# Performance work log

Hardware: AMD Instinct MI355X
Metric: run time of the kernel (lower is better)

## Reference

```python
import jax, jax.numpy as jnp
import numpy as np

N_HEAD = 16
NEG = -10000.0


def setup_inputs() -> dict:
    key = jax.random.key(0)
    k1, k2, k3 = jax.random.split(key, 3)
    B, S, NX = 2, 2048, 1024
    x = jax.random.normal(k1, (B, S, NX), dtype=jnp.float32)
    # Conv1D weights: y = x @ W + b (HF Conv1D stores weight as [in, out])
    w_attn = jax.random.normal(k2, (NX, 3 * NX), dtype=jnp.float32) * 0.02
    b_attn = jnp.zeros((3 * NX,), dtype=jnp.float32)
    w_proj = jax.random.normal(k3, (NX, NX), dtype=jnp.float32) * 0.02
    b_proj = jnp.zeros((NX,), dtype=jnp.float32)
    return {"x": x, "w_attn": w_attn, "b_attn": b_attn,
            "w_proj": w_proj, "b_proj": b_proj}


def reference(x, w_attn, b_attn, w_proj, b_proj):
    B, S, NX = x.shape
    H = N_HEAD
    D = NX // H  # head dim
    qkv = x @ w_attn + b_attn                      # [B, S, 3*NX]
    q, k, v = jnp.split(qkv, 3, axis=-1)
    # split heads -> [B, H, S, D]
    q = q.reshape(B, S, H, D).transpose(0, 2, 1, 3)
    k = k.reshape(B, S, H, D).transpose(0, 2, 1, 3)
    v = v.reshape(B, S, H, D).transpose(0, 2, 1, 3)
    # scores [B, H, S, S], scaled (scale=True)
    w = jnp.einsum('bhqd,bhkd->bhqk', q, k) / jnp.sqrt(jnp.asarray(D, x.dtype))
    # causal additive mask exactly as the torch code: w*b + NEG*(1-b)
    bias = jnp.tril(jnp.ones((S, S), dtype=x.dtype))[None, None]  # [1,1,S,S]
    w = w * bias + NEG * (1.0 - bias)
    w = jax.nn.softmax(w, axis=-1)
    a = jnp.einsum('bhqk,bhkd->bhqd', w, v)        # [B, H, S, D]
    a = a.transpose(0, 2, 1, 3).reshape(B, S, NX)  # merge heads
    return a @ w_proj + b_proj
```

## Files before the change

kernel.cpp:

```cpp
#include <hip/hip_runtime.h>
#include <cstdint>
#include <cstddef>


typedef __bf16 bf16;
typedef __bf16 bf16x8 __attribute__((ext_vector_type(8)));
typedef __bf16 bf16x4 __attribute__((ext_vector_type(4)));
typedef float f32x4 __attribute__((ext_vector_type(4)));
typedef float f32x16 __attribute__((ext_vector_type(16)));

#define MFMA16(a, b, c) __builtin_amdgcn_mfma_f32_16x16x32_bf16(a, b, c, 0, 0, 0)
#define MFMA32(a, b, c) __builtin_amdgcn_mfma_f32_32x32x16_bf16(a, b, c, 0, 0, 0)

typedef const __attribute__((address_space(1))) void* gas_ptr;
typedef __attribute__((address_space(3))) void* las_ptr;
__device__ __forceinline__ void async16(const void* g, void* l) {
    __builtin_amdgcn_global_load_lds((gas_ptr)g, (las_ptr)l, 16, 0, 0);
}
__device__ __forceinline__ float exp2f_fast(float x) { return __builtin_amdgcn_exp2f(x); }
__device__ __forceinline__ uint32_t pkbf(float a, float b) {
    union { bf16 x[2]; uint32_t u; } t;
    t.x[0] = (bf16)a; t.x[1] = (bf16)b;
    return t.u;
}

__global__ __launch_bounds__(256) void prep_kernel(const float* __restrict__ x, bf16* __restrict__ xb,
                                                   const float* __restrict__ wa, bf16* __restrict__ wTa,
                                                   const float* __restrict__ wp, bf16* __restrict__ wTp) {
    __shared__ float tile[32][33];
    const int bid = blockIdx.x, tid = threadIdx.x;
    if (bid < 4096) {
        int i = (bid * 256 + tid) * 4;
        float4 v = *reinterpret_cast<const float4*>(x + i);
        bf16x4 o;
        o[0] = (bf16)v.x; o[1] = (bf16)v.y; o[2] = (bf16)v.z; o[3] = (bf16)v.w;
        *reinterpret_cast<bf16x4*>(xb + i) = o;
        return;
    }
    const float* in; bf16* out; int N, t;
    if (bid < 7168) { t = bid - 4096; in = wa; out = wTa; N = 3072; }
    else            { t = bid - 7168; in = wp; out = wTp; N = 1024; }
    const int K = 1024;
    int bx = t % (N >> 5), by = t / (N >> 5);
    int n0 = bx * 32, k0 = by * 32, tx = tid & 31, ty = tid >> 5;
#pragma unroll
    for (int i = 0; i < 32; i += 8)
        tile[ty + i][tx] = in[(size_t)(k0 + ty + i) * N + n0 + tx];
    __syncthreads();
#pragma unroll
    for (int i = 0; i < 32; i += 8)
        out[(size_t)(n0 + ty + i) * K + k0 + tx] = (bf16)tile[tx][ty + i];
}

template <int OUT_BF16>
__global__ __launch_bounds__(256) void gemm_kernel(const bf16* __restrict__ A,
                                                   const bf16* __restrict__ Bt,
                                                   const float* __restrict__ bias,
                                                   void* __restrict__ Cout,
                                                   int M, int N, int K) {
    __shared__ bf16 Alds[2][128 * 32];
    __shared__ bf16 Blds[2][128 * 32];
    const int tid = threadIdx.x;
    const int w = tid >> 6, l = tid & 63;
    const int lane16 = l & 15, quad = l >> 4;
    const int wr = w >> 1, wc = w & 1;

    const int nwg = gridDim.x * gridDim.y;
    const int lin = blockIdx.x + gridDim.x * blockIdx.y;
    const int q8 = nwg >> 3;
    const int swz = (lin & 7) * q8 + (lin >> 3);
    const int bx = swz % gridDim.x, by = swz / gridDim.x;
    const int row0 = by * 128, col0 = bx * 128;

    int grs[2], gks[2];
#pragma unroll
    for (int c = 0; c < 2; ++c) {
        int idx = c * 256 + tid;
        int R = idx >> 3, pos = idx & 7;
        int pos2 = pos ^ (R & 7);
        grs[c] = 2 * R + (pos2 >> 2);
        gks[c] = (pos2 & 3) * 8;
    }

    f32x4 zero4 = {0.f, 0.f, 0.f, 0.f};
    f32x4 acc[4][4];
#pragma unroll
    for (int i = 0; i < 4; ++i)
#pragma unroll
        for (int j = 0; j < 4; ++j) acc[i][j] = zero4;

    auto stage = [&](int buf, int k0) {
#pragma unroll
        for (int c = 0; c < 2; ++c) {
            int idx = c * 256 + tid;
            async16(A + (size_t)(row0 + grs[c]) * K + k0 + gks[c], &Alds[buf][idx * 8]);
            async16(Bt + (size_t)(col0 + grs[c]) * K + k0 + gks[c], &Blds[buf][idx * 8]);
        }
    };

    stage(0, 0);
    const int niter = K >> 5;
    for (int it = 0; it < niter; ++it) {
        const int cur = it & 1;
        __syncthreads();
        if (it + 1 < niter) stage(cur ^ 1, (it + 1) << 5);
        bf16x8 af[4], bfr[4];
#pragma unroll
        for (int i = 0; i < 4; ++i) {
            int gra = 64 * wr + 16 * i + lane16;
            int Ra = gra >> 1;
            int pa = ((gra & 1) * 4 + quad) ^ (Ra & 7);
            af[i] = *reinterpret_cast<const bf16x8*>(&Alds[cur][Ra * 64 + pa * 8]);
            int grb = 64 * wc + 16 * i + lane16;
            int Rb = grb >> 1;
            int pb = ((grb & 1) * 4 + quad) ^ (Rb & 7);
            bfr[i] = *reinterpret_cast<const bf16x8*>(&Blds[cur][Rb * 64 + pb * 8]);
        }
#pragma unroll
        for (int i = 0; i < 4; ++i)
#pragma unroll
            for (int j = 0; j < 4; ++j) acc[i][j] = MFMA16(af[i], bfr[j], acc[i][j]);
    }

#pragma unroll
    for (int i = 0; i < 4; ++i)
#pragma unroll
        for (int j = 0; j < 4; ++j)
#pragma unroll
            for (int r = 0; r < 4; ++r) {
                int row = row0 + 64 * wr + 16 * i + quad * 4 + r;
                int col = col0 + 64 * wc + 16 * j + lane16;
                float v = acc[i][j][r] + bias[col];
                if (OUT_BF16)
                    reinterpret_cast<bf16*>(Cout)[(size_t)row * N + col] = (bf16)v;
                else
                    reinterpret_cast<float*>(Cout)[(size_t)row * N + col] = v;
            }
}

template <int OUT_BF16>
__global__ __launch_bounds__(256) void gemm64k_kernel(const bf16* __restrict__ A,
                                                      const bf16* __restrict__ Bt,
                                                      const float* __restrict__ bias,
                                                      void* __restrict__ Cout,
                                                      int M, int N, int K) {
    __shared__ bf16 Alds[2][64 * 64];
    __shared__ bf16 Blds[2][128 * 64];
    const int tid = threadIdx.x;
    const int w = tid >> 6, l = tid & 63;
    const int lane16 = l & 15, quad = l >> 4;
    const int wr = w >> 1, wc = w & 1;
    const int row0 = blockIdx.y * 64, col0 = blockIdx.x * 128;

    f32x4 zero4 = {0.f, 0.f, 0.f, 0.f};
    f32x4 acc[2][4];
#pragma unroll
    for (int i = 0; i < 2; ++i)
#pragma unroll
        for (int j = 0; j < 4; ++j) acc[i][j] = zero4;

    auto stage = [&](int buf, int k0) {
#pragma unroll
        for (int c = 0; c < 2; ++c) {
            int idx = c * 256 + tid;
            int r = idx >> 3, cc = idx & 7, gc = cc ^ (r & 7);
            async16(A + (size_t)(row0 + r) * K + k0 + gc * 8, &Alds[buf][idx * 8]);
        }
#pragma unroll
        for (int c = 0; c < 4; ++c) {
            int idx = c * 256 + tid;
            int r = idx >> 3, cc = idx & 7, gc = cc ^ (r & 7);
            async16(Bt + (size_t)(col0 + r) * K + k0 + gc * 8, &Blds[buf][idx * 8]);
        }
    };

    stage(0, 0);
    const int niter = K >> 6;
    for (int it = 0; it < niter; ++it) {
        const int cur = it & 1;
        __syncthreads();
        if (it + 1 < niter) stage(cur ^ 1, (it + 1) << 6);
        bf16x8 af[2][2], bfr[4][2];
#pragma unroll
        for (int i = 0; i < 2; ++i) {
            int r = 32 * wr + 16 * i + lane16;
#pragma unroll
            for (int ks = 0; ks < 2; ++ks) {
                int cc = (quad + 4 * ks) ^ (r & 7);
                af[i][ks] = *reinterpret_cast<const bf16x8*>(&Alds[cur][r * 64 + cc * 8]);
            }
        }
#pragma unroll
        for (int j = 0; j < 4; ++j) {
            int r = 64 * wc + 16 * j + lane16;
#pragma unroll
            for (int ks = 0; ks < 2; ++ks) {
                int cc = (quad + 4 * ks) ^ (r & 7);
                bfr[j][ks] = *reinterpret_cast<const bf16x8*>(&Blds[cur][r * 64 + cc * 8]);
            }
        }
#pragma unroll
        for (int ks = 0; ks < 2; ++ks)
#pragma unroll
            for (int i = 0; i < 2; ++i)
#pragma unroll
                for (int j = 0; j < 4; ++j) acc[i][j] = MFMA16(af[i][ks], bfr[j][ks], acc[i][j]);
    }

#pragma unroll
    for (int i = 0; i < 2; ++i)
#pragma unroll
        for (int j = 0; j < 4; ++j)
#pragma unroll
            for (int r = 0; r < 4; ++r) {
                int row = row0 + 32 * wr + 16 * i + quad * 4 + r;
                int col = col0 + 64 * wc + 16 * j + lane16;
                float v = acc[i][j][r] + bias[col];
                if (OUT_BF16)
                    reinterpret_cast<bf16*>(Cout)[(size_t)row * N + col] = (bf16)v;
                else
                    reinterpret_cast<float*>(Cout)[(size_t)row * N + col] = v;
            }
}

__global__ __launch_bounds__(256, 4) void attn_kernel(const bf16* __restrict__ qkv,
                                                      bf16* __restrict__ aout) {
    const int S = 2048;
    const int bh = blockIdx.x;
    const int b = bh >> 4, hd = bh & 15;
    const int rr = blockIdx.y >> 3, j = blockIdx.y & 7;
    const int qt = (rr == 0) ? (31 - j) : (rr == 1) ? (16 + j) : (rr == 2) ? (15 - j) : j;
    const int nkt = qt + 1;
    const int tid = threadIdx.x, w = tid >> 6, l = tid & 63;
    const int lane32 = l & 31, h = l >> 5;
    const int qh = w & 1, kh = w >> 1;

    __shared__ bf16 Klds[2][64 * 64];
    __shared__ bf16 Vt[2][64 * 64];
    __shared__ float Lbuf[2][2][32];

    const bf16* base = qkv + (size_t)b * S * 3072;
    const float qscale = 0.125f * 1.4426950408889634f;
    const float NEGs = -10000.0f * 1.4426950408889634f;

    bf16x8 qf[4];
    {
        const bf16* qp = base + (size_t)(qt * 64 + qh * 32 + lane32) * 3072 + hd * 64;
#pragma unroll
        for (int s = 0; s < 4; ++s) {
            bf16x8 t = *reinterpret_cast<const bf16x8*>(qp + s * 16 + h * 8);
#pragma unroll
            for (int jj = 0; jj < 8; ++jj) t[jj] = (bf16)((float)t[jj] * qscale);
            qf[s] = t;
        }
    }

    f32x16 oacc[2];
#pragma unroll
    for (int dt = 0; dt < 2; ++dt)
#pragma unroll
        for (int i = 0; i < 16; ++i) oacc[dt][i] = 0.f;
    float lsum = 0.f;

    const int kr = tid >> 3, kcc = tid & 7;
    const int vp = tid & 31, vd = (tid >> 5) * 8;
    bf16x8 kreg0, kreg1, vreg0, vreg1;
    auto load_tile = [&](int kt) {
        const bf16* tb = base + (size_t)(kt * 64) * 3072;
        kreg0 = *reinterpret_cast<const bf16x8*>(tb + (size_t)kr * 3072 + 1024 + hd * 64 + kcc * 8);
        kreg1 = *reinterpret_cast<const bf16x8*>(tb + (size_t)(32 + kr) * 3072 + 1024 + hd * 64 + kcc * 8);
        vreg0 = *reinterpret_cast<const bf16x8*>(tb + (size_t)(2 * vp) * 3072 + 2048 + hd * 64 + vd);
        vreg1 = *reinterpret_cast<const bf16x8*>(tb + (size_t)(2 * vp + 1) * 3072 + 2048 + hd * 64 + vd);
    };
    auto write_KV = [&](int buf) {
        bf16* Kb = &Klds[buf][0];
        bf16* Vb = &Vt[buf][0];
        const int kchunk = kcc ^ (kr & 7);
        *reinterpret_cast<bf16x8*>(&Kb[kr * 64 + kchunk * 8]) = kreg0;
        *reinterpret_cast<bf16x8*>(&Kb[(32 + kr) * 64 + kchunk * 8]) = kreg1;
#pragma unroll
        for (int jj = 0; jj < 8; ++jj) {
            int row = vd + jj;
            union { bf16 h2v[2]; uint32_t u; } pk;
            pk.h2v[0] = vreg0[jj]; pk.h2v[1] = vreg1[jj];
            int idx = row * 64 + (((vp >> 2) ^ (row & 7)) * 8) + (vp & 3) * 2;
            *reinterpret_cast<uint32_t*>(&Vb[idx]) = pk.u;
        }
    };

    load_tile(0);
    write_KV(0);
    if (nkt > 1) load_tile(1);
    __syncthreads();

    const int krow = kh * 32 + lane32;
    for (int kt = 0; kt < nkt; ++kt) {
        const int p = kt & 1;
        if (kt + 1 < nkt) write_KV(p ^ 1);

        f32x16 st;
#pragma unroll
        for (int i = 0; i < 16; ++i) st[i] = 0.f;
        __builtin_amdgcn_s_setprio(1);
#pragma unroll
        for (int s = 0; s < 4; ++s) {
            int ch = (2 * s + h) ^ (krow & 7);
            bf16x8 kf = *reinterpret_cast<const bf16x8*>(&Klds[p][krow * 64 + ch * 8]);
            st = MFMA32(kf, qf[s], st);
        }
        __builtin_amdgcn_s_setprio(0);

        if (kt + 2 < nkt) load_tile(kt + 2);

        if (kt == qt) {
            const int q = qh * 32 + lane32;
#pragma unroll
            for (int reg = 0; reg < 16; ++reg) {
                int kloc = kh * 32 + 4 * h + (reg & 3) + 8 * (reg >> 2);
                if (kloc > q) st[reg] = NEGs;
            }
        }

        uint32_t wpk[4][2];
        float rs = 0.f;
#pragma unroll
        for (int g = 0; g < 4; ++g) {
            float p0 = exp2f_fast(st[4 * g + 0]);
            float p1 = exp2f_fast(st[4 * g + 1]);
            float p2 = exp2f_fast(st[4 * g + 2]);
            float p3 = exp2f_fast(st[4 * g + 3]);
            rs += (p0 + p1) + (p2 + p3);
            wpk[g][0] = pkbf(p0, p1);
            wpk[g][1] = pkbf(p2, p3);
        }
        lsum += rs;

        uint32_t opk[4][2];
#pragma unroll
        for (int g = 0; g < 4; ++g) {
            opk[g][0] = (uint32_t)__shfl_xor((int)wpk[g][0], 32, 64);
            opk[g][1] = (uint32_t)__shfl_xor((int)wpk[g][1], 32, 64);
        }

        bf16x8 pf[2];
#pragma unroll
        for (int s2 = 0; s2 < 2; ++s2) {
            union { uint32_t u[4]; bf16x8 v; } pu;
            const int g0 = 2 * s2, g1 = 2 * s2 + 1;
            pu.u[0] = h ? opk[g1][0] : wpk[g0][0];
            pu.u[1] = h ? opk[g1][1] : wpk[g0][1];
            pu.u[2] = h ? wpk[g1][0] : opk[g0][0];
            pu.u[3] = h ? wpk[g1][1] : opk[g0][1];
            pf[s2] = pu.v;
        }

        __builtin_amdgcn_s_setprio(1);
#pragma unroll
        for (int dt = 0; dt < 2; ++dt) {
            int vrow = dt * 32 + lane32;
#pragma unroll
            for (int s2 = 0; s2 < 2; ++s2) {
                int kc = (4 * kh + 2 * s2 + h) ^ (vrow & 7);
                bf16x8 vf = *reinterpret_cast<const bf16x8*>(&Vt[p][vrow * 64 + kc * 8]);
                oacc[dt] = MFMA32(pf[s2], vf, oacc[dt]);
            }
        }
        __builtin_amdgcn_s_setprio(0);

        __syncthreads();
    }

    lsum += __shfl_xor(lsum, 32, 64);
    if (l < 32) Lbuf[kh][qh][lane32] = lsum;

    float* Obuf = reinterpret_cast<float*>(&Klds[0][0]);
    if (kh == 1) {
#pragma unroll
        for (int dt = 0; dt < 2; ++dt)
#pragma unroll
            for (int reg = 0; reg < 16; ++reg) {
                int qrow = (reg & 3) + 8 * (reg >> 2) + 4 * h;
                Obuf[(qh * 32 + qrow) * 64 + dt * 32 + lane32] = oacc[dt][reg];
            }
    }
    __syncthreads();

    if (kh == 0) {
        float linv[16];
#pragma unroll
        for (int reg = 0; reg < 16; ++reg) {
            int qrow = (reg & 3) + 8 * (reg >> 2) + 4 * h;
            linv[reg] = 1.0f / (Lbuf[0][qh][qrow] + Lbuf[1][qh][qrow]);
        }
#pragma unroll
        for (int dt = 0; dt < 2; ++dt)
#pragma unroll
            for (int reg = 0; reg < 16; ++reg) {
                int qrow = (reg & 3) + 8 * (reg >> 2) + 4 * h;
                float v = (oacc[dt][reg] + Obuf[(qh * 32 + qrow) * 64 + dt * 32 + lane32]) * linv[reg];
                aout[(size_t)(b * S + qt * 64 + qh * 32 + qrow) * 1024 + hd * 64 + dt * 32 + lane32] =
                    (bf16)v;
            }
    }
}

extern "C" void kernel_launch(void* const* d_in, const int* in_sizes, int n_in,
                              void* d_out, int out_size, void* d_ws, size_t ws_size,
                              hipStream_t stream) {
    const float* x      = (const float*)d_in[0];
    const float* w_attn = (const float*)d_in[1];
    const float* b_attn = (const float*)d_in[2];
    const float* w_proj = (const float*)d_in[3];
    const float* b_proj = (const float*)d_in[4];
    float* out = (float*)d_out;
    char* ws = (char*)d_ws;

    const int Mtok = 4096, NX = 1024, N3 = 3072;
    bf16* xb   = (bf16*)(ws);
    bf16* wTa  = (bf16*)(ws + ((size_t)8 << 20));
    bf16* wTp  = (bf16*)(ws + ((size_t)14 << 20));
    bf16* qkv  = (bf16*)(ws + ((size_t)16 << 20));
    bf16* abuf = (bf16*)(ws + ((size_t)40 << 20));

    prep_kernel<<<dim3(8192), 256, 0, stream>>>(x, xb, w_attn, wTa, w_proj, wTp);
    gemm_kernel<1><<<dim3(N3 / 128, Mtok / 128), 256, 0, stream>>>(xb, wTa, b_attn, qkv, Mtok, N3, NX);
    attn_kernel<<<dim3(32, 32), 256, 0, stream>>>(qkv, abuf);
    gemm64k_kernel<0><<<dim3(NX / 128, Mtok / 64), 256, 0, stream>>>(abuf, wTp, b_proj, out, Mtok, NX, NX);
}
```

Measured before the change: 168.5 us.

## Fuse x conversion into QKV GEMM, split-K output projection, shrink attention LDS

The fp32-to-bf16 conversion of x moves out of the prep kernel and into the QKV GEMM, which loads fp32 A tiles into registers and converts them while writing LDS. This removes a separate pass over x and the bf16 staging buffer. The output projection switches from a 64x128 tile kernel to a 128x128 split-K=2 kernel that writes two fp32 partial buffers, and a new add kernel sums them. The attention kernel packs its shared memory into one aliased 32KB buffer and raises occupancy to 5 blocks per unit. In exchange it adds an extra launch and extra fp32 traffic for the partials, and the A loads are now synchronous register loads rather than async copies.

After: 262.5 us. 55.8% more time.

```diff
diff --git a/kernel.cpp b/kernel.cpp
--- a/kernel.cpp
+++ b/kernel.cpp
@@ -24,22 +24,13 @@
     return t.u;
 }
 
-__global__ __launch_bounds__(256) void prep_kernel(const float* __restrict__ x, bf16* __restrict__ xb,
-                                                   const float* __restrict__ wa, bf16* __restrict__ wTa,
+__global__ __launch_bounds__(256) void prep_kernel(const float* __restrict__ wa, bf16* __restrict__ wTa,
                                                    const float* __restrict__ wp, bf16* __restrict__ wTp) {
     __shared__ float tile[32][33];
     const int bid = blockIdx.x, tid = threadIdx.x;
-    if (bid < 4096) {
-        int i = (bid * 256 + tid) * 4;
-        float4 v = *reinterpret_cast<const float4*>(x + i);
-        bf16x4 o;
-        o[0] = (bf16)v.x; o[1] = (bf16)v.y; o[2] = (bf16)v.z; o[3] = (bf16)v.w;
-        *reinterpret_cast<bf16x4*>(xb + i) = o;
-        return;
-    }
     const float* in; bf16* out; int N, t;
-    if (bid < 7168) { t = bid - 4096; in = wa; out = wTa; N = 3072; }
-    else            { t = bid - 7168; in = wp; out = wTp; N = 1024; }
+    if (bid < 3072) { t = bid;        in = wa; out = wTa; N = 3072; }
+    else            { t = bid - 3072; in = wp; out = wTp; N = 1024; }
     const int K = 1024;
     int bx = t % (N >> 5), by = t / (N >> 5);
     int n0 = bx * 32, k0 = by * 32, tx = tid & 31, ty = tid >> 5;
@@ -52,12 +43,11 @@
         out[(size_t)(n0 + ty + i) * K + k0 + tx] = (bf16)tile[tx][ty + i];
 }
 
-template <int OUT_BF16>
-__global__ __launch_bounds__(256) void gemm_kernel(const bf16* __restrict__ A,
-                                                   const bf16* __restrict__ Bt,
-                                                   const float* __restrict__ bias,
-                                                   void* __restrict__ Cout,
-                                                   int M, int N, int K) {
+__global__ __launch_bounds__(256) void gemmx_kernel(const float* __restrict__ X,
+                                                    const bf16* __restrict__ Bt,
+                                                    const float* __restrict__ bias,
+                                                    bf16* __restrict__ Cout,
+                                                    int M, int N, int K) {
     __shared__ bf16 Alds[2][128 * 32];
     __shared__ bf16 Blds[2][128 * 32];
     const int tid = threadIdx.x;
@@ -89,21 +79,49 @@
 #pragma unroll
         for (int j = 0; j < 4; ++j) acc[i][j] = zero4;
 
-    auto stage = [&](int buf, int k0) {
+    f32x4 areg[4];
+    auto loadA = [&](int k0) {
+#pragma unroll
+        for (int c = 0; c < 2; ++c) {
+            const float* src = X + (size_t)(row0 + grs[c]) * K + k0 + gks[c];
+            areg[2 * c]     = *reinterpret_cast<const f32x4*>(src);
+            areg[2 * c + 1] = *reinterpret_cast<const f32x4*>(src + 4);
+        }
+    };
+    auto writeA = [&](int buf) {
 #pragma unroll
         for (int c = 0; c < 2; ++c) {
             int idx = c * 256 + tid;
-            async16(A + (size_t)(row0 + grs[c]) * K + k0 + gks[c], &Alds[buf][idx * 8]);
+            bf16x8 o;
+#pragma unroll
+            for (int e = 0; e < 4; ++e) {
+                o[e]     = (bf16)areg[2 * c][e];
+                o[e + 4] = (bf16)areg[2 * c + 1][e];
+            }
+            *reinterpret_cast<bf16x8*>(&Alds[buf][idx * 8]) = o;
+        }
+    };
+    auto stageB = [&](int buf, int k0) {
+#pragma unroll
+        for (int c = 0; c < 2; ++c) {
+            int idx = c * 256 + tid;
             async16(Bt + (size_t)(col0 + grs[c]) * K + k0 + gks[c], &Blds[buf][idx * 8]);
         }
     };
 
-    stage(0, 0);
+    loadA(0);
+    writeA(0);
+    stageB(0, 0);
+    loadA(32);
     const int niter = K >> 5;
     for (int it = 0; it < niter; ++it) {
         const int cur = it & 1;
         __syncthreads();
-        if (it + 1 < niter) stage(cur ^ 1, (it + 1) << 5);
+        if (it + 1 < niter) {
+            writeA(cur ^ 1);
+            stageB(cur ^ 1, (it + 1) << 5);
+            if (it + 2 < niter) loadA((it + 2) << 5);
+        }
         bf16x8 af[4], bfr[4];
 #pragma unroll
         for (int i = 0; i < 4; ++i) {
@@ -130,32 +148,46 @@
             for (int r = 0; r < 4; ++r) {
                 int row = row0 + 64 * wr + 16 * i + quad * 4 + r;
                 int col = col0 + 64 * wc + 16 * j + lane16;
-                float v = acc[i][j][r] + bias[col];
-                if (OUT_BF16)
-                    reinterpret_cast<bf16*>(Cout)[(size_t)row * N + col] = (bf16)v;
-                else
-                    reinterpret_cast<float*>(Cout)[(size_t)row * N + col] = v;
-            }
-}
-
-template <int OUT_BF16>
-__global__ __launch_bounds__(256) void gemm64k_kernel(const bf16* __restrict__ A,
-                                                      const bf16* __restrict__ Bt,
-                                                      const float* __restrict__ bias,
-                                                      void* __restrict__ Cout,
-                                                      int M, int N, int K) {
-    __shared__ bf16 Alds[2][64 * 64];
-    __shared__ bf16 Blds[2][128 * 64];
+                Cout[(size_t)row * N + col] = (bf16)(acc[i][j][r] + bias[col]);
+            }
+}
+
+__global__ __launch_bounds__(256) void gemm_splitk_kernel(const bf16* __restrict__ A,
+                                                          const bf16* __restrict__ Bt,
+                                                          const float* __restrict__ bias,
+                                                          float* __restrict__ P0,
+                                                          float* __restrict__ P1,
+                                                          int M, int N, int K) {
+    __shared__ bf16 Alds[2][128 * 32];
+    __shared__ bf16 Blds[2][128 * 32];
     const int tid = threadIdx.x;
     const int w = tid >> 6, l = tid & 63;
     const int lane16 = l & 15, quad = l >> 4;
     const int wr = w >> 1, wc = w & 1;
-    const int row0 = blockIdx.y * 64, col0 = blockIdx.x * 128;
+    const int kz = blockIdx.z;
+    const int kbase = kz * (K >> 1);
+
+    const int nwg = gridDim.x * gridDim.y;
+    const int lin = blockIdx.x + gridDim.x * blockIdx.y;
+    const int q8 = nwg >> 3;
+    const int swz = (lin & 7) * q8 + (lin >> 3);
+    const int bx = swz % gridDim.x, by = swz / gridDim.x;
+    const int row0 = by * 128, col0 = bx * 128;
+
+    int grs[2], gks[2];
+#pragma unroll
+    for (int c = 0; c < 2; ++c) {
+        int idx = c * 256 + tid;
+        int R = idx >> 3, pos = idx & 7;
+        int pos2 = pos ^ (R & 7);
+        grs[c] = 2 * R + (pos2 >> 2);
+        gks[c] = (pos2 & 3) * 8;
+    }
 
     f32x4 zero4 = {0.f, 0.f, 0.f, 0.f};
-    f32x4 acc[2][4];
-#pragma unroll
-    for (int i = 0; i < 2; ++i)
+    f32x4 acc[4][4];
+#pragma unroll
+    for (int i = 0; i < 4; ++i)
 #pragma unroll
         for (int j = 0; j < 4; ++j) acc[i][j] = zero4;
 
@@ -163,67 +195,58 @@
 #pragma unroll
         for (int c = 0; c < 2; ++c) {
             int idx = c * 256 + tid;
-            int r = idx >> 3, cc = idx & 7, gc = cc ^ (r & 7);
-            async16(A + (size_t)(row0 + r) * K + k0 + gc * 8, &Alds[buf][idx * 8]);
-        }
-#pragma unroll
-        for (int c = 0; c < 4; ++c) {
-            int idx = c * 256 + tid;
-            int r = idx >> 3, cc = idx & 7, gc = cc ^ (r & 7);
-            async16(Bt + (size_t)(col0 + r) * K + k0 + gc * 8, &Blds[buf][idx * 8]);
-        }
-    };
-
-    stage(0, 0);
+            async16(A + (size_t)(row0 + grs[c]) * K + k0 + gks[c], &Alds[buf][idx * 8]);
+            async16(Bt + (size_t)(col0 + grs[c]) * K + k0 + gks[c], &Blds[buf][idx * 8]);
+        }
+    };
+
+    stage(0, kbase);
     const int niter = K >> 6;
     for (int it = 0; it < niter; ++it) {
         const int cur = it & 1;
         __syncthreads();
-        if (it + 1 < niter) stage(cur ^ 1, (it + 1) << 6);
-        bf16x8 af[2][2], bfr[4][2];
-#pragma unroll
-        for (int i = 0; i < 2; ++i) {
-            int r = 32 * wr + 16 * i + lane16;
-#pragma unroll
-            for (int ks = 0; ks < 2; ++ks) {
-                int cc = (quad + 4 * ks) ^ (r & 7);
-                af[i][ks] = *reinterpret_cast<const bf16x8*>(&Alds[cur][r * 64 + cc * 8]);
-            }
-        }
-#pragma unroll
-        for (int j = 0; j < 4; ++j) {
-            int r = 64 * wc + 16 * j + lane16;
-#pragma unroll
-            for (int ks = 0; ks < 2; ++ks) {
-                int cc = (quad + 4 * ks) ^ (r & 7);
-                bfr[j][ks] = *reinterpret_cast<const bf16x8*>(&Blds[cur][r * 64 + cc * 8]);
-            }
-        }
-#pragma unroll
-        for (int ks = 0; ks < 2; ++ks)
-#pragma unroll
-            for (int i = 0; i < 2; ++i)
-#pragma unroll
-                for (int j = 0; j < 4; ++j) acc[i][j] = MFMA16(af[i][ks], bfr[j][ks], acc[i][j]);
-    }
-
-#pragma unroll
-    for (int i = 0; i < 2; ++i)
+        if (it + 1 < niter) stage(cur ^ 1, kbase + ((it + 1) << 5));
+        bf16x8 af[4], bfr[4];
+#pragma unroll
+        for (int i = 0; i < 4; ++i) {
+            int gra = 64 * wr + 16 * i + lane16;
+            int Ra = gra >> 1;
+            int pa = ((gra & 1) * 4 + quad) ^ (Ra & 7);
+            af[i] = *reinterpret_cast<const bf16x8*>(&Alds[cur][Ra * 64 + pa * 8]);
+            int grb = 64 * wc + 16 * i + lane16;
+            int Rb = grb >> 1;
+            int pb = ((grb & 1) * 4 + quad) ^ (Rb & 7);
+            bfr[i] = *reinterpret_cast<const bf16x8*>(&Blds[cur][Rb * 64 + pb * 8]);
+        }
+#pragma unroll
+        for (int i = 0; i < 4; ++i)
+#pragma unroll
+            for (int j = 0; j < 4; ++j) acc[i][j] = MFMA16(af[i], bfr[j], acc[i][j]);
+    }
+
+    float* P = kz ? P1 : P0;
+#pragma unroll
+    for (int i = 0; i < 4; ++i)
 #pragma unroll
         for (int j = 0; j < 4; ++j)
 #pragma unroll
             for (int r = 0; r < 4; ++r) {
-                int row = row0 + 32 * wr + 16 * i + quad * 4 + r;
+                int row = row0 + 64 * wr + 16 * i + quad * 4 + r;
                 int col = col0 + 64 * wc + 16 * j + lane16;
-                float v = acc[i][j][r] + bias[col];
-                if (OUT_BF16)
-                    reinterpret_cast<bf16*>(Cout)[(size_t)row * N + col] = (bf16)v;
-                else
-                    reinterpret_cast<float*>(Cout)[(size_t)row * N + col] = v;
-            }
-}
-
-__global__ __launch_bounds__(256, 4) void attn_kernel(const bf16* __restrict__ qkv,
+                float v = acc[i][j][r] + (kz == 0 ? bias[col] : 0.f);
+                P[(size_t)row * N + col] = v;
+            }
+}
+
+__global__ __launch_bounds__(256) void add2_kernel(const f32x4* __restrict__ p0,
+                                                   const f32x4* __restrict__ p1,
+                                                   f32x4* __restrict__ o) {
+    int i = (blockIdx.x * 256 + threadIdx.x) * 2;
+    o[i]     = p0[i]     + p1[i];
+    o[i + 1] = p0[i + 1] + p1[i + 1];
+}
+
+__global__ __launch_bounds__(256, 5) void attn_kernel(const bf16* __restrict__ qkv,
                                                       bf16* __restrict__ aout) {
     const int S = 2048;
     const int bh = blockIdx.x;
@@ -235,9 +258,11 @@
     const int lane32 = l & 31, h = l >> 5;
     const int qh = w & 1, kh = w >> 1;
 
-    __shared__ bf16 Klds[2][64 * 64];
-    __shared__ bf16 Vt[2][64 * 64];
-    __shared__ float Lbuf[2][2][32];
+    __shared__ __align__(16) char smem[32768];
+    bf16* Ksh = reinterpret_cast<bf16*>(smem);
+    bf16* Vsh = reinterpret_cast<bf16*>(smem + 16384);
+    float* Obuf = reinterpret_cast<float*>(smem);
+    float* Lb = reinterpret_cast<float*>(smem + 16384);
 
     const bf16* base = qkv + (size_t)b * S * 3072;
     const float qscale = 0.125f * 1.4426950408889634f;
@@ -273,8 +298,8 @@
         vreg1 = *reinterpret_cast<const bf16x8*>(tb + (size_t)(2 * vp + 1) * 3072 + 2048 + hd * 64 + vd);
     };
     auto write_KV = [&](int buf) {
-        bf16* Kb = &Klds[buf][0];
-        bf16* Vb = &Vt[buf][0];
+        bf16* Kb = Ksh + buf * 4096;
+        bf16* Vb = Vsh + buf * 4096;
         const int kchunk = kcc ^ (kr & 7);
         *reinterpret_cast<bf16x8*>(&Kb[kr * 64 + kchunk * 8]) = kreg0;
         *reinterpret_cast<bf16x8*>(&Kb[(32 + kr) * 64 + kchunk * 8]) = kreg1;
@@ -305,7 +330,7 @@
 #pragma unroll
         for (int s = 0; s < 4; ++s) {
             int ch = (2 * s + h) ^ (krow & 7);
-            bf16x8 kf = *reinterpret_cast<const bf16x8*>(&Klds[p][krow * 64 + ch * 8]);
+            bf16x8 kf = *reinterpret_cast<const bf16x8*>(&Ksh[p * 4096 + krow * 64 + ch * 8]);
             st = MFMA32(kf, qf[s], st);
         }
         __builtin_amdgcn_s_setprio(0);
@@ -361,7 +386,7 @@
 #pragma unroll
             for (int s2 = 0; s2 < 2; ++s2) {
                 int kc = (4 * kh + 2 * s2 + h) ^ (vrow & 7);
-                bf16x8 vf = *reinterpret_cast<const bf16x8*>(&Vt[p][vrow * 64 + kc * 8]);
+                bf16x8 vf = *reinterpret_cast<const bf16x8*>(&Vsh[p * 4096 + vrow * 64 + kc * 8]);
                 oacc[dt] = MFMA32(pf[s2], vf, oacc[dt]);
             }
         }
@@ -371,9 +396,8 @@
     }
 
     lsum += __shfl_xor(lsum, 32, 64);
-    if (l < 32) Lbuf[kh][qh][lane32] = lsum;
-
-    float* Obuf = reinterpret_cast<float*>(&Klds[0][0]);
+    if (l < 32) Lb[(kh * 2 + qh) * 32 + lane32] = lsum;
+
     if (kh == 1) {
 #pragma unroll
         for (int dt = 0; dt < 2; ++dt)
@@ -390,7 +414,7 @@
 #pragma unroll
         for (int reg = 0; reg < 16; ++reg) {
             int qrow = (reg & 3) + 8 * (reg >> 2) + 4 * h;
-            linv[reg] = 1.0f / (Lbuf[0][qh][qrow] + Lbuf[1][qh][qrow]);
+            linv[reg] = 1.0f / (Lb[(0 * 2 + qh) * 32 + qrow] + Lb[(1 * 2 + qh) * 32 + qrow]);
         }
 #pragma unroll
         for (int dt = 0; dt < 2; ++dt)
@@ -416,14 +440,16 @@
     char* ws = (char*)d_ws;
 
     const int Mtok = 4096, NX = 1024, N3 = 3072;
-    bf16* xb   = (bf16*)(ws);
     bf16* wTa  = (bf16*)(ws + ((size_t)8 << 20));
     bf16* wTp  = (bf16*)(ws + ((size_t)14 << 20));
     bf16* qkv  = (bf16*)(ws + ((size_t)16 << 20));
     bf16* abuf = (bf16*)(ws + ((size_t)40 << 20));
-
-    prep_kernel<<<dim3(8192), 256, 0, stream>>>(x, xb, w_attn, wTa, w_proj, wTp);
-    gemm_kernel<1><<<dim3(N3 / 128, Mtok / 128), 256, 0, stream>>>(xb, wTa, b_attn, qkv, Mtok, N3, NX);
+    float* p0  = (float*)(ws + ((size_t)48 << 20));
+    float* p1  = (float*)(ws + ((size_t)64 << 20));
+
+    prep_kernel<<<dim3(4096), 256, 0, stream>>>(w_attn, wTa, w_proj, wTp);
+    gemmx_kernel<<<dim3(N3 / 128, Mtok / 128), 256, 0, stream>>>(x, wTa, b_attn, qkv, Mtok, N3, NX);
     attn_kernel<<<dim3(32, 32), 256, 0, stream>>>(qkv, abuf);
-    gemm64k_kernel<0><<<dim3(NX / 128, Mtok / 64), 256, 0, stream>>>(abuf, wTp, b_proj, out, Mtok, NX, NX);
-}
+    gemm_splitk_kernel<<<dim3(NX / 128, Mtok / 128, 2), 256, 0, stream>>>(abuf, wTp, b_proj, p0, p1, Mtok, NX, NX);
+    add2_kernel<<<dim3(2048), 256, 0, stream>>>((const f32x4*)p0, (const f32x4*)p1, (f32x4*)out);
+}
```
